# Optimization experiments

Measured on AMD Instinct MI355X. Metric: run time of the kernel, lower is better.

## Reference

```python
import jax, jax.numpy as jnp
import numpy as np
from math import sqrt

B, TS_D, SEG, D, H, FACTOR, DFF = 16, 32, 64, 256, 8, 10, 1024
EPS = 1e-3  # keras LayerNormalization default epsilon


def _dense_params(key, din, dout):
    return (jax.random.normal(key, (din, dout), jnp.float32) * 0.02,
            jnp.zeros((dout,), jnp.float32))


def setup_inputs() -> dict:
    key = jax.random.key(0)
    ks = jax.random.split(key, 32)
    inp = {"x": jax.random.normal(ks[0], (B, TS_D, SEG, D), jnp.float32)}
    inp["router"] = jax.random.normal(ks[1], (SEG, FACTOR, D), jnp.float32) * 0.02
    i = 2
    for pref in ["t", "s", "r"]:  # time_attention, dim_sender, dim_receiver
        for nm in ["q", "k", "v", "o"]:
            w, b = _dense_params(ks[i], D, D); i += 1
            inp[pref + nm + "_w"] = w
            inp[pref + nm + "_b"] = b
    for j in range(1, 5):
        inp["n%d_g" % j] = jnp.ones((D,), jnp.float32)
        inp["n%d_b" % j] = jnp.zeros((D,), jnp.float32)
    for pref in ["m1", "m2"]:
        w1, b1 = _dense_params(ks[i], D, DFF); i += 1
        w2, b2 = _dense_params(ks[i], DFF, D); i += 1
        inp[pref + "w1"] = w1; inp[pref + "b1"] = b1
        inp[pref + "w2"] = w2; inp[pref + "b2"] = b2
    return inp


def _attn(q, k, v, wq, bq, wk, bk, wv, bv, wo, bo):
    # multi-head full attention; dropout is identity at inference
    Bq, L, _ = q.shape
    S = k.shape[1]
    E = D // H
    qh = (q @ wq + bq).reshape(Bq, L, H, E)
    kh = (k @ wk + bk).reshape(Bq, S, H, E)
    vh = (v @ wv + bv).reshape(Bq, S, H, E)
    scores = jnp.einsum('blhe,bshe->bhls', qh, kh) * (1.0 / sqrt(E))
    A = jax.nn.softmax(scores, axis=-1)
    out = jnp.einsum('bhls,bshd->blhd', A, vh).reshape(Bq, L, H * E)
    return out @ wo + bo


def _ln(x, g, b):
    m = jnp.mean(x, axis=-1, keepdims=True)
    v = jnp.mean(jnp.square(x - m), axis=-1, keepdims=True)
    return (x - m) / jnp.sqrt(v + EPS) * g + b


def _mlp(x, w1, b1, w2, b2):
    return jax.nn.gelu(x @ w1 + b1, approximate=False) @ w2 + b2


def reference(x, router, tq_w, tq_b, tk_w, tk_b, tv_w, tv_b, to_w, to_b,
              sq_w, sq_b, sk_w, sk_b, sv_w, sv_b, so_w, so_b,
              rq_w, rq_b, rk_w, rk_b, rv_w, rv_b, ro_w, ro_b,
              n1_g, n1_b, n2_g, n2_b, n3_g, n3_b, n4_g, n4_b,
              m1w1, m1b1, m1w2, m1b2, m2w1, m2b1, m2w2, m2b2):
    b, ts_d, seg, d = x.shape
    # ---- stage 1: attention across time segments (per variable) ----
    time_in = x.reshape(b * ts_d, seg, d)
    time_enc = _attn(time_in, time_in, time_in,
                     tq_w, tq_b, tk_w, tk_b, tv_w, tv_b, to_w, to_b)
    dim_in = _ln(time_in + time_enc, n1_g, n1_b)
    dim_in = _ln(dim_in + _mlp(dim_in, m1w1, m1b1, m1w2, m1b2), n2_g, n2_b)
    # ---- stage 2: routed attention across variable dimension (per segment) ----
    # '(b ts_d) seg d -> (b seg) ts_d d'
    dim_send = dim_in.reshape(b, ts_d, seg, d).transpose(0, 2, 1, 3).reshape(b * seg, ts_d, d)
    # tf.repeat(router, repeats=batch, axis=0): each segment's router repeated b times (seg-major)
    batch_router = jnp.repeat(router, b, axis=0)  # (seg*b, factor, d)
    dim_buffer = _attn(batch_router, dim_send, dim_send,
                       sq_w, sq_b, sk_w, sk_b, sv_w, sv_b, so_w, so_b)
    dim_receive = _attn(dim_send, dim_buffer, dim_buffer,
                        rq_w, rq_b, rk_w, rk_b, rv_w, rv_b, ro_w, ro_b)
    dim_enc = _ln(dim_send + dim_receive, n3_g, n3_b)
    dim_enc = _ln(dim_enc + _mlp(dim_enc, m2w1, m2b1, m2w2, m2b2), n4_g, n4_b)
    # '(b seg) ts_d d -> b ts_d seg d'
    return dim_enc.reshape(b, seg, ts_d, d).transpose(0, 2, 1, 3)
```

## Files before the change

kernel.cpp:

```cpp
#include <hip/hip_runtime.h>
#include <hip/hip_bf16.h>

#define DIM   256
#define NH    8
#define HE    32
#define ROWS  32768
#define EPS_LN 1e-3f

typedef float f32x4 __attribute__((ext_vector_type(4)));
typedef short s16x8 __attribute__((ext_vector_type(8)));
typedef short s16x4 __attribute__((ext_vector_type(4)));
typedef __bf16 bf16x8 __attribute__((ext_vector_type(8)));

__device__ __forceinline__ unsigned short f2bf(float f){
    union { float f; unsigned int u; } v; v.f = f;
    unsigned int u = v.u;
    return (unsigned short)((u + 0x7fffu + ((u >> 16) & 1u)) >> 16);
}

__device__ __forceinline__ float gelu_f(float x){
    return 0.5f * x * (1.0f + erff(x * 0.70710678118654752440f));
}

__device__ __forceinline__ void mfma16i(f32x4& acc, s16x8 a, s16x8 b){
    acc = __builtin_amdgcn_mfma_f32_16x16x32_bf16(
        __builtin_bit_cast(bf16x8, a), __builtin_bit_cast(bf16x8, b), acc, 0, 0, 0);
}

__device__ __forceinline__ s16x8 pack8(float4 a, float4 b){
    s16x8 v;
    v[0]=(short)f2bf(a.x); v[1]=(short)f2bf(a.y);
    v[2]=(short)f2bf(a.z); v[3]=(short)f2bf(a.w);
    v[4]=(short)f2bf(b.x); v[5]=(short)f2bf(b.y);
    v[6]=(short)f2bf(b.z); v[7]=(short)f2bf(b.w);
    return v;
}

__device__ __forceinline__ void gld16(const unsigned short* g, unsigned short* l){
    __builtin_amdgcn_global_load_lds(
        (const __attribute__((address_space(1))) unsigned int*)g,
        (__attribute__((address_space(3))) unsigned int*)l, 16, 0, 0);
}

struct WtArgs { const float* w[16]; unsigned short* o[16]; };
__global__ __launch_bounds__(256) void transp_all_k(WtArgs a){
    int idx = blockIdx.x * 256 + threadIdx.x;
    int wi, rem, K, N;
    if (idx < 786432){ wi = idx >> 16; rem = idx & 65535; K = 256; N = 256; }
    else { int t = idx - 786432; wi = 12 + (t >> 18); rem = t & 262143;
           if ((wi & 1) == 0){ K = 256; N = 1024; } else { K = 1024; N = 256; } }
    int ln = (N == 256) ? 8 : 10;
    int k = rem >> ln, n = rem & (N - 1);
    a.o[wi][n * K + k] = f2bf(a.w[wi][rem]);
}

struct BcArgs { const float* src[8]; float* dst; };
__global__ __launch_bounds__(256) void bias_cat_k(BcArgs a){
    int idx = blockIdx.x * 256 + threadIdx.x;
    a.dst[idx] = a.src[idx >> 8][idx & 255];
}

template<int ACT, int ABF16, int CBF16, int SPLIT>
__global__ __launch_bounds__(256) void gemm_k(const void* __restrict__ Av,
        const unsigned short* __restrict__ Wt, const float* __restrict__ bias,
        void* C0, void* C1, void* C2, int M, int N, int K){
    __shared__ __align__(16) unsigned short As[2][128 * 32];
    __shared__ __align__(16) unsigned short Bs[2][128 * 32];
    const int tid  = threadIdx.x;
    const long row0 = (long)blockIdx.x * 128;
    const long col0 = (long)blockIdx.y * 128;
    const int w = tid >> 6, lane = tid & 63;
    const int wm = w >> 1, wn = w & 1;
    const int l15 = lane & 15, g = lane >> 4;
    const unsigned short* Bg = Wt + (size_t)(col0 + 32 * w + (lane >> 2)) * K + (lane & 3) * 8;
    const int sr = tid >> 1, sk = (tid & 1) << 4;
    const float* Ap = (const float*)Av + (size_t)(row0 + sr) * K + sk;
    const unsigned short* Ag = (const unsigned short*)Av +
        (size_t)(row0 + 32 * w + (lane >> 2)) * K + (lane & 3) * 8;

    auto stage = [&](int kk, int nb){
        gld16(Bg + kk, &Bs[nb][(32 * w) * 32]);
        gld16(Bg + 16 * K + kk, &Bs[nb][(32 * w + 16) * 32]);
        if (ABF16){
            gld16(Ag + kk, &As[nb][(32 * w) * 32]);
            gld16(Ag + 16 * K + kk, &As[nb][(32 * w + 16) * 32]);
        } else {
            float4 a0 = *(const float4*)(Ap + kk);
            float4 a1 = *(const float4*)(Ap + kk + 4);
            float4 a2 = *(const float4*)(Ap + kk + 8);
            float4 a3 = *(const float4*)(Ap + kk + 12);
            *(s16x8*)&As[nb][sr * 32 + sk]     = pack8(a0, a1);
            *(s16x8*)&As[nb][sr * 32 + sk + 8] = pack8(a2, a3);
        }
    };

    f32x4 acc[4][4];
    #pragma unroll
    for (int i = 0; i < 4; i++)
        #pragma unroll
        for (int jj = 0; jj < 4; jj++) acc[i][jj] = (f32x4){0,0,0,0};

    stage(0, 0);
    __syncthreads();
    int cur = 0;
    for (int k0 = 0; k0 < K; k0 += 32){
        if (k0 + 32 < K) stage(k0 + 32, cur ^ 1);
        s16x8 af[4], bf[4];
        #pragma unroll
        for (int mi = 0; mi < 4; mi++)
            af[mi] = *(const s16x8*)&As[cur][(wm * 64 + mi * 16 + l15) * 32 + g * 8];
        #pragma unroll
        for (int ni = 0; ni < 4; ni++)
            bf[ni] = *(const s16x8*)&Bs[cur][(wn * 64 + ni * 16 + l15) * 32 + g * 8];
        #pragma unroll
        for (int mi = 0; mi < 4; mi++)
            #pragma unroll
            for (int ni = 0; ni < 4; ni++)
                mfma16i(acc[mi][ni], af[mi], bf[ni]);
        __syncthreads();
        cur ^= 1;
    }
    const int sel = SPLIT ? (int)(col0 >> 8) : 0;
    void* Cp = SPLIT ? (sel == 0 ? C0 : (sel == 1 ? C1 : C2)) : C0;
    const int ldc = SPLIT ? 256 : N;
    float bb[4];
    #pragma unroll
    for (int ni = 0; ni < 4; ni++) bb[ni] = bias[col0 + wn * 64 + ni * 16 + l15];
    #pragma unroll
    for (int mi = 0; mi < 4; mi++){
        const long grow = row0 + wm * 64 + mi * 16 + g * 4;
        #pragma unroll
        for (int ni = 0; ni < 4; ni++){
            int gcol = (int)col0 + wn * 64 + ni * 16 + l15;
            int lcol = SPLIT ? (gcol & 255) : gcol;
            #pragma unroll
            for (int r = 0; r < 4; r++){
                float v = acc[mi][ni][r] + bb[ni];
                if (ACT) v = gelu_f(v);
                if (CBF16) ((unsigned short*)Cp)[(grow + r) * ldc + lcol] = f2bf(v);
                else       ((float*)Cp)[(grow + r) * ldc + lcol] = v;
            }
        }
    }
}

__global__ __launch_bounds__(64) void attn64_k(const float* __restrict__ Q,
        const float* __restrict__ Kp, const float* __restrict__ Vp,
        float* __restrict__ O){
    __shared__ __align__(16) unsigned short P[64][72];
    const int j = blockIdx.x >> 3, h = blockIdx.x & 7;
    const int lane = threadIdx.x;
    const int l15 = lane & 15, g = lane >> 4;
    const long base = (long)j * 64 * DIM;
    const int hoff = h * HE;
    const float scale = 0.17677669529663687f;
    s16x8 kf[4], qf[4];
    #pragma unroll
    for (int b = 0; b < 4; b++){
        const float* kp = Kp + base + (long)(b * 16 + l15) * DIM + hoff + g * 8;
        kf[b] = pack8(*(const float4*)kp, *(const float4*)(kp + 4));
        const float* qp = Q + base + (long)(b * 16 + l15) * DIM + hoff + g * 8;
        qf[b] = pack8(*(const float4*)qp, *(const float4*)(qp + 4));
    }
    f32x4 st[4][4];
    #pragma unroll
    for (int sb = 0; sb < 4; sb++)
        #pragma unroll
        for (int qb = 0; qb < 4; qb++) st[sb][qb] = (f32x4){0,0,0,0};
    #pragma unroll
    for (int sb = 0; sb < 4; sb++)
        #pragma unroll
        for (int qb = 0; qb < 4; qb++) mfma16i(st[sb][qb], kf[sb], qf[qb]);
    #pragma unroll
    for (int sb = 0; sb < 4; sb++)
        #pragma unroll
        for (int qb = 0; qb < 4; qb++)
            #pragma unroll
            for (int r = 0; r < 4; r++) st[sb][qb][r] *= scale;
    #pragma unroll
    for (int qb = 0; qb < 4; qb++){
        float mx = -1e30f;
        #pragma unroll
        for (int sb = 0; sb < 4; sb++)
            #pragma unroll
            for (int r = 0; r < 4; r++) mx = fmaxf(mx, st[sb][qb][r]);
        mx = fmaxf(mx, __shfl_xor(mx, 16, 64));
        mx = fmaxf(mx, __shfl_xor(mx, 32, 64));
        float sum = 0.f;
        #pragma unroll
        for (int sb = 0; sb < 4; sb++)
            #pragma unroll
            for (int r = 0; r < 4; r++){
                float e = expf(st[sb][qb][r] - mx);
                st[sb][qb][r] = e; sum += e;
            }
        sum += __shfl_xor(sum, 16, 64);
        sum += __shfl_xor(sum, 32, 64);
        float inv = 1.f / sum;
        const int q = qb * 16 + l15;
        #pragma unroll
        for (int sb = 0; sb < 4; sb++){
            s16x4 p4;
            #pragma unroll
            for (int r = 0; r < 4; r++) p4[r] = (short)f2bf(st[sb][qb][r] * inv);
            *(s16x4*)&P[q][sb * 16 + g * 4] = p4;
        }
    }
    __syncthreads();
    f32x4 o[4][2];
    #pragma unroll
    for (int qb = 0; qb < 4; qb++)
        #pragma unroll
        for (int eb = 0; eb < 2; eb++) o[qb][eb] = (f32x4){0,0,0,0};
    #pragma unroll
    for (int ksl = 0; ksl < 2; ksl++){
        s16x8 pf[4], vf[2];
        #pragma unroll
        for (int qb = 0; qb < 4; qb++)
            pf[qb] = *(const s16x8*)&P[qb * 16 + l15][ksl * 32 + g * 8];
        #pragma unroll
        for (int eb = 0; eb < 2; eb++){
            const float* vp = Vp + base + (long)(ksl * 32 + g * 8) * DIM + hoff + eb * 16 + l15;
            s16x8 vv;
            #pragma unroll
            for (int jj = 0; jj < 8; jj++) vv[jj] = (short)f2bf(vp[(long)jj * DIM]);
            vf[eb] = vv;
        }
        #pragma unroll
        for (int qb = 0; qb < 4; qb++)
            #pragma unroll
            for (int eb = 0; eb < 2; eb++) mfma16i(o[qb][eb], pf[qb], vf[eb]);
    }
    #pragma unroll
    for (int qb = 0; qb < 4; qb++)
        #pragma unroll
        for (int eb = 0; eb < 2; eb++){
            const int q = qb * 16 + g * 4;
            float* op = O + base + (long)q * DIM + hoff + eb * 16 + l15;
            #pragma unroll
            for (int r = 0; r < 4; r++) op[(long)r * DIM] = o[qb][eb][r];
        }
}

template<int L, int S, int QMODE>
__global__ __launch_bounds__(256) void attn_k(const float* __restrict__ Q,
        const float* __restrict__ Kp, const float* __restrict__ Vp,
        float* __restrict__ O){
    __shared__ float Qs[L][36];
    __shared__ float Ks[S][36];
    __shared__ float Vs[S][36];
    __shared__ float Sc[L][S + 1];
    const int j = blockIdx.x >> 3, h = blockIdx.x & 7;
    const int tid = threadIdx.x;
    const long qbase = QMODE ? (long)(j >> 4) * L : (long)j * L;
    const long kbase = (long)j * S;
    const long obase = (long)j * L;
    const int hoff = h * HE;
    for (int idx = tid; idx < L * 8; idx += 256){
        int i = idx >> 3, e4 = (idx & 7) << 2;
        *reinterpret_cast<float4*>(&Qs[i][e4]) =
            *reinterpret_cast<const float4*>(Q + (qbase + i) * DIM + hoff + e4);
    }
    for (int idx = tid; idx < S * 8; idx += 256){
        int i = idx >> 3, e4 = (idx & 7) << 2;
        *reinterpret_cast<float4*>(&Ks[i][e4]) =
            *reinterpret_cast<const float4*>(Kp + (kbase + i) * DIM + hoff + e4);
        *reinterpret_cast<float4*>(&Vs[i][e4]) =
            *reinterpret_cast<const float4*>(Vp + (kbase + i) * DIM + hoff + e4);
    }
    __syncthreads();
    for (int idx = tid; idx < L * S; idx += 256){
        int i = idx / S, jj = idx % S;
        float d = 0.f;
        #pragma unroll
        for (int q4 = 0; q4 < 8; q4++){
            float4 a = *reinterpret_cast<const float4*>(&Qs[i][q4 * 4]);
            float4 b = *reinterpret_cast<const float4*>(&Ks[jj][q4 * 4]);
            d += a.x * b.x + a.y * b.y + a.z * b.z + a.w * b.w;
        }
        Sc[i][jj] = d * 0.17677669529663687f;
    }
    __syncthreads();
    if (tid < L){
        float mx = -1e30f;
        for (int jj = 0; jj < S; jj++) mx = fmaxf(mx, Sc[tid][jj]);
        float s = 0.f;
        for (int jj = 0; jj < S; jj++){ float e = expf(Sc[tid][jj] - mx); Sc[tid][jj] = e; s += e; }
        float inv = 1.f / s;
        for (int jj = 0; jj < S; jj++) Sc[tid][jj] *= inv;
    }
    __syncthreads();
    for (int idx = tid; idx < L * 8; idx += 256){
        int i = idx >> 3, e4 = (idx & 7) << 2;
        float4 o = {0.f, 0.f, 0.f, 0.f};
        for (int jj = 0; jj < S; jj++){
            float s = Sc[i][jj];
            float4 v = *reinterpret_cast<const float4*>(&Vs[jj][e4]);
            o.x += s * v.x; o.y += s * v.y; o.z += s * v.z; o.w += s * v.w;
        }
        *reinterpret_cast<float4*>(O + (obase + i) * DIM + hoff + e4) = o;
    }
}

template<int PERM>
__global__ __launch_bounds__(256) void ln_k(const float* __restrict__ X,
        const float* __restrict__ R, const float* __restrict__ g,
        const float* __restrict__ be, float* __restrict__ Y){
    const int wid = threadIdx.x >> 6, lane = threadIdx.x & 63;
    const long row = (long)blockIdx.x * 4 + wid;
    float4 xv = *reinterpret_cast<const float4*>(X + row * DIM + lane * 4);
    float4 rv = *reinterpret_cast<const float4*>(R + row * DIM + lane * 4);
    float4 v = {xv.x + rv.x, xv.y + rv.y, xv.z + rv.z, xv.w + rv.w};
    float s = v.x + v.y + v.z + v.w;
    #pragma unroll
    for (int m = 1; m < 64; m <<= 1) s += __shfl_xor(s, m, 64);
    float mean = s * (1.f / 256.f);
    float dx = v.x - mean, dy = v.y - mean, dz = v.z - mean, dw = v.w - mean;
    float q = dx * dx + dy * dy + dz * dz + dw * dw;
    #pragma unroll
    for (int m = 1; m < 64; m <<= 1) q += __shfl_xor(q, m, 64);
    float rstd = rsqrtf(q * (1.f / 256.f) + EPS_LN);
    float4 gv = *reinterpret_cast<const float4*>(g  + lane * 4);
    float4 bv = *reinterpret_cast<const float4*>(be + lane * 4);
    long rout = row;
    if (PERM == 1){ int b = (int)(row >> 11), rem = (int)row & 2047, t = rem >> 6, sg = rem & 63;
                    rout = (long)b * 2048 + sg * 32 + t; }
    if (PERM == 2){ int b = (int)(row >> 11), rem = (int)row & 2047, sg = rem >> 5, t = rem & 31;
                    rout = (long)b * 2048 + t * 64 + sg; }
    float4 o = { dx * rstd * gv.x + bv.x, dy * rstd * gv.y + bv.y,
                 dz * rstd * gv.z + bv.z, dw * rstd * gv.w + bv.w };
    *reinterpret_cast<float4*>(Y + rout * DIM + lane * 4) = o;
}

extern "C" void kernel_launch(void* const* d_in, const int* in_sizes, int n_in,
                              void* d_out, int out_size, void* d_ws, size_t ws_size,
                              hipStream_t stream){
    const float* x      = (const float*)d_in[0];
    const float* router = (const float*)d_in[1];
    const float* n1g = (const float*)d_in[26]; const float* n1b = (const float*)d_in[27];
    const float* n2g = (const float*)d_in[28]; const float* n2b = (const float*)d_in[29];
    const float* n3g = (const float*)d_in[30]; const float* n3b = (const float*)d_in[31];
    const float* n4g = (const float*)d_in[32]; const float* n4b = (const float*)d_in[33];

    char* ws = (char*)d_ws;
    const size_t ACTB = (size_t)ROWS * DIM * 4;
    float* buf0 = (float*)(ws);
    float* buf1 = (float*)(ws + 1 * ACTB);
    float* buf2 = (float*)(ws + 2 * ACTB);
    float* buf3 = (float*)(ws + 3 * ACTB);
    float* buf4 = (float*)(ws + 4 * ACTB);
    float* buf5 = (float*)(ws + 5 * ACTB);
    unsigned short* bufH16 = (unsigned short*)buf0;
    size_t off = 6 * ACTB;
    float* bufS1 = (float*)(ws + off); off += (size_t)10240 * 256 * 4;
    float* bufS2 = (float*)(ws + off); off += (size_t)10240 * 256 * 4;
    float* bufR  = (float*)(ws + off); off += (size_t)640 * 256 * 4;
    float* bcat  = (float*)(ws + off); off += 2048 * 4;
    unsigned short* wtbase = (unsigned short*)(ws + off);

    const int wsel[16] = {2,4,6, 12,14,18, 20,22, 8,10,16,24, 34,36,38,40};
    unsigned short* wt[16];
    { size_t o = 0;
      for (int i = 0; i < 12; i++){ wt[i] = wtbase + o; o += 65536; }
      for (int i = 12; i < 16; i++){ wt[i] = wtbase + o; o += 262144; } }
    WtArgs wa;
    for (int i = 0; i < 16; i++){ wa.w[i] = (const float*)d_in[wsel[i]]; wa.o[i] = wt[i]; }
    transp_all_k<<<7168, 256, 0, stream>>>(wa);
    BcArgs ba;
    { const int bs[8] = {3,5,7, 13,15,19, 21,23};
      for (int i = 0; i < 8; i++) ba.src[i] = (const float*)d_in[bs[i]];
      ba.dst = bcat; }
    bias_cat_k<<<8, 256, 0, stream>>>(ba);

    const unsigned short *G0 = wt[0], *G1 = wt[3], *G2 = wt[6];
    const unsigned short *Wto = wt[8], *Wsq = wt[9], *Wso = wt[10], *Wro = wt[11];
    const unsigned short *Wm1a = wt[12], *Wm1b = wt[13], *Wm2a = wt[14], *Wm2b = wt[15];
    const float* b_to = (const float*)d_in[9];  const float* b_sq = (const float*)d_in[11];
    const float* b_so = (const float*)d_in[17]; const float* b_ro = (const float*)d_in[25];
    const float* m1b1 = (const float*)d_in[35]; const float* m1b2 = (const float*)d_in[37];
    const float* m2b1 = (const float*)d_in[39]; const float* m2b2 = (const float*)d_in[41];

    gemm_k<0,0,0,1><<<dim3(256,6), 256, 0, stream>>>(x, G0, bcat,
        buf0, buf1, buf2, ROWS, 768, 256);
    attn64_k<<<dim3(512 * 8), 64, 0, stream>>>(buf0, buf1, buf2, buf3);
    gemm_k<0,0,0,0><<<dim3(256,2), 256, 0, stream>>>(buf3, Wto, b_to,
        buf5, nullptr, nullptr, ROWS, 256, 256);
    ln_k<0><<<ROWS / 4, 256, 0, stream>>>(buf5, x, n1g, n1b, buf4);
    gemm_k<1,0,1,0><<<dim3(256,8), 256, 0, stream>>>(buf4, Wm1a, m1b1,
        bufH16, nullptr, nullptr, ROWS, 1024, 256);
    gemm_k<0,1,0,0><<<dim3(256,2), 256, 0, stream>>>(bufH16, Wm1b, m1b2,
        buf5, nullptr, nullptr, ROWS, 256, 1024);
    ln_k<1><<<ROWS / 4, 256, 0, stream>>>(buf5, buf4, n2g, n2b, buf0);

    gemm_k<0,0,0,0><<<dim3(5,2), 256, 0, stream>>>(router, Wsq, b_sq,
        bufR, nullptr, nullptr, 640, 256, 256);
    gemm_k<0,0,0,1><<<dim3(256,6), 256, 0, stream>>>(buf0, G1, bcat + 768,
        buf1, buf2, buf3, ROWS, 768, 256);
    attn_k<10,32,1><<<dim3(1024 * 8), 256, 0, stream>>>(bufR, buf1, buf2, bufS1);
    gemm_k<0,0,0,0><<<dim3(80,2), 256, 0, stream>>>(bufS1, Wso, b_so,
        bufS2, nullptr, nullptr, 10240, 256, 256);
    gemm_k<0,0,0,1><<<dim3(80,4), 256, 0, stream>>>(bufS2, G2, bcat + 1536,
        bufS1, buf1, nullptr, 10240, 512, 256);
    attn_k<32,10,0><<<dim3(1024 * 8), 256, 0, stream>>>(buf3, bufS1, buf1, buf2);
    gemm_k<0,0,0,0><<<dim3(256,2), 256, 0, stream>>>(buf2, Wro, b_ro,
        buf3, nullptr, nullptr, ROWS, 256, 256);
    ln_k<0><<<ROWS / 4, 256, 0, stream>>>(buf3, buf0, n3g, n3b, buf4);
    gemm_k<1,0,1,0><<<dim3(256,8), 256, 0, stream>>>(buf4, Wm2a, m2b1,
        bufH16, nullptr, nullptr, ROWS, 1024, 256);
    gemm_k<0,1,0,0><<<dim3(256,2), 256, 0, stream>>>(bufH16, Wm2b, m2b2,
        buf5, nullptr, nullptr, ROWS, 256, 1024);
    ln_k<2><<<ROWS / 4, 256, 0, stream>>>(buf5, buf4, n4g, n4b, (float*)d_out);
}
```

Measured before the change: 617.7 us.

## Store all intermediate activations in bf16 and swizzle GEMM LDS tiles

Every intermediate activation buffer (QKV projections, attention outputs, LayerNorm outputs, GEMM outputs) is now stored in bf16 instead of fp32. This roughly halves activation memory traffic between the many kernels, and the input x and router are converted to bf16 once up front. The GEMM now always loads A directly to LDS via global_load_lds, uses an XOR swizzle to avoid bank conflicts, and replaces __syncthreads with explicit vmcnt waits and s_barrier. The added bf16 rounding of residuals and LayerNorm inputs reduces accuracy.

```diff
diff --git a/kernel.cpp b/kernel.cpp
--- a/kernel.cpp
+++ b/kernel.cpp
@@ -17,29 +17,32 @@
     unsigned int u = v.u;
     return (unsigned short)((u + 0x7fffu + ((u >> 16) & 1u)) >> 16);
 }
-
+__device__ __forceinline__ float bf2f(unsigned short u){
+    union { unsigned int i; float f; } v; v.i = (unsigned int)u << 16; return v.f;
+}
 __device__ __forceinline__ float gelu_f(float x){
     return 0.5f * x * (1.0f + erff(x * 0.70710678118654752440f));
 }
-
 __device__ __forceinline__ void mfma16i(f32x4& acc, s16x8 a, s16x8 b){
     acc = __builtin_amdgcn_mfma_f32_16x16x32_bf16(
         __builtin_bit_cast(bf16x8, a), __builtin_bit_cast(bf16x8, b), acc, 0, 0, 0);
 }
-
-__device__ __forceinline__ s16x8 pack8(float4 a, float4 b){
-    s16x8 v;
-    v[0]=(short)f2bf(a.x); v[1]=(short)f2bf(a.y);
-    v[2]=(short)f2bf(a.z); v[3]=(short)f2bf(a.w);
-    v[4]=(short)f2bf(b.x); v[5]=(short)f2bf(b.y);
-    v[6]=(short)f2bf(b.z); v[7]=(short)f2bf(b.w);
-    return v;
-}
-
 __device__ __forceinline__ void gld16(const unsigned short* g, unsigned short* l){
     __builtin_amdgcn_global_load_lds(
         (const __attribute__((address_space(1))) unsigned int*)g,
         (__attribute__((address_space(3))) unsigned int*)l, 16, 0, 0);
+}
+
+__global__ __launch_bounds__(256) void conv_k(const float* __restrict__ in,
+        unsigned short* __restrict__ out, int n8){
+    int idx = blockIdx.x * 256 + threadIdx.x;
+    if (idx >= n8) return;
+    const float4 a = *(const float4*)(in + idx * 8);
+    const float4 b = *(const float4*)(in + idx * 8 + 4);
+    s16x8 v;
+    v[0]=(short)f2bf(a.x); v[1]=(short)f2bf(a.y); v[2]=(short)f2bf(a.z); v[3]=(short)f2bf(a.w);
+    v[4]=(short)f2bf(b.x); v[5]=(short)f2bf(b.y); v[6]=(short)f2bf(b.z); v[7]=(short)f2bf(b.w);
+    *(s16x8*)(out + idx * 8) = v;
 }
 
 struct WtArgs { const float* w[16]; unsigned short* o[16]; };
@@ -60,10 +63,11 @@
     a.dst[idx] = a.src[idx >> 8][idx & 255];
 }
 
-template<int ACT, int ABF16, int CBF16, int SPLIT>
-__global__ __launch_bounds__(256) void gemm_k(const void* __restrict__ Av,
+template<int ACT, int SPLIT>
+__global__ __launch_bounds__(256) void gemm_k(const unsigned short* __restrict__ A,
         const unsigned short* __restrict__ Wt, const float* __restrict__ bias,
-        void* C0, void* C1, void* C2, int M, int N, int K){
+        unsigned short* C0, unsigned short* C1, unsigned short* C2,
+        int M, int N, int K){
     __shared__ __align__(16) unsigned short As[2][128 * 32];
     __shared__ __align__(16) unsigned short Bs[2][128 * 32];
     const int tid  = threadIdx.x;
@@ -72,56 +76,55 @@
     const int w = tid >> 6, lane = tid & 63;
     const int wm = w >> 1, wn = w & 1;
     const int l15 = lane & 15, g = lane >> 4;
-    const unsigned short* Bg = Wt + (size_t)(col0 + 32 * w + (lane >> 2)) * K + (lane & 3) * 8;
-    const int sr = tid >> 1, sk = (tid & 1) << 4;
-    const float* Ap = (const float*)Av + (size_t)(row0 + sr) * K + sk;
-    const unsigned short* Ag = (const unsigned short*)Av +
-        (size_t)(row0 + 32 * w + (lane >> 2)) * K + (lane & 3) * 8;
-
-    auto stage = [&](int kk, int nb){
-        gld16(Bg + kk, &Bs[nb][(32 * w) * 32]);
-        gld16(Bg + 16 * K + kk, &Bs[nb][(32 * w + 16) * 32]);
-        if (ABF16){
-            gld16(Ag + kk, &As[nb][(32 * w) * 32]);
-            gld16(Ag + 16 * K + kk, &As[nb][(32 * w + 16) * 32]);
+    const int jsrc = ((lane & 3) ^ ((lane >> 3) & 3)) * 8;
+    const unsigned short* Ag = A  + (size_t)(row0 + 32 * w + (lane >> 2)) * K + jsrc;
+    const unsigned short* Bg = Wt + (size_t)(col0 + 32 * w + (lane >> 2)) * K + jsrc;
+    unsigned short* Al0[2] = { &As[0][(32 * w) * 32], &As[1][(32 * w) * 32] };
+    unsigned short* Bl0[2] = { &Bs[0][(32 * w) * 32], &Bs[1][(32 * w) * 32] };
+
+    f32x4 acc[4][4];
+    #pragma unroll
+    for (int i = 0; i < 4; i++)
+        #pragma unroll
+        for (int jj = 0; jj < 4; jj++) acc[i][jj] = (f32x4){0,0,0,0};
+
+    const int NT = K >> 5;
+    gld16(Ag, Al0[0]);          gld16(Ag + 16 * K, Al0[0] + 16 * 32);
+    gld16(Bg, Bl0[0]);          gld16(Bg + 16 * K, Bl0[0] + 16 * 32);
+    for (int t = 0; t < NT; ++t){
+        const int cur = t & 1;
+        if (t + 1 < NT){
+            const int kk = (t + 1) << 5;
+            gld16(Ag + kk, Al0[cur ^ 1]);  gld16(Ag + kk + 16 * K, Al0[cur ^ 1] + 16 * 32);
+            gld16(Bg + kk, Bl0[cur ^ 1]);  gld16(Bg + kk + 16 * K, Bl0[cur ^ 1] + 16 * 32);
+            asm volatile("s_waitcnt vmcnt(4)" ::: "memory");
         } else {
-            float4 a0 = *(const float4*)(Ap + kk);
-            float4 a1 = *(const float4*)(Ap + kk + 4);
-            float4 a2 = *(const float4*)(Ap + kk + 8);
-            float4 a3 = *(const float4*)(Ap + kk + 12);
-            *(s16x8*)&As[nb][sr * 32 + sk]     = pack8(a0, a1);
-            *(s16x8*)&As[nb][sr * 32 + sk + 8] = pack8(a2, a3);
-        }
-    };
-
-    f32x4 acc[4][4];
-    #pragma unroll
-    for (int i = 0; i < 4; i++)
-        #pragma unroll
-        for (int jj = 0; jj < 4; jj++) acc[i][jj] = (f32x4){0,0,0,0};
-
-    stage(0, 0);
-    __syncthreads();
-    int cur = 0;
-    for (int k0 = 0; k0 < K; k0 += 32){
-        if (k0 + 32 < K) stage(k0 + 32, cur ^ 1);
+            asm volatile("s_waitcnt vmcnt(0)" ::: "memory");
+        }
+        __builtin_amdgcn_sched_barrier(0);
+        __builtin_amdgcn_s_barrier();
+        __builtin_amdgcn_sched_barrier(0);
         s16x8 af[4], bf[4];
         #pragma unroll
-        for (int mi = 0; mi < 4; mi++)
-            af[mi] = *(const s16x8*)&As[cur][(wm * 64 + mi * 16 + l15) * 32 + g * 8];
-        #pragma unroll
-        for (int ni = 0; ni < 4; ni++)
-            bf[ni] = *(const s16x8*)&Bs[cur][(wn * 64 + ni * 16 + l15) * 32 + g * 8];
+        for (int mi = 0; mi < 4; mi++){
+            const int r = mi * 16 + l15;
+            af[mi] = *(const s16x8*)&As[cur][(wm * 64 + r) * 32 + ((g ^ ((l15 >> 1) & 3)) * 8)];
+        }
+        #pragma unroll
+        for (int ni = 0; ni < 4; ni++){
+            const int r = ni * 16 + l15;
+            bf[ni] = *(const s16x8*)&Bs[cur][(wn * 64 + r) * 32 + ((g ^ ((l15 >> 1) & 3)) * 8)];
+        }
         #pragma unroll
         for (int mi = 0; mi < 4; mi++)
             #pragma unroll
             for (int ni = 0; ni < 4; ni++)
                 mfma16i(acc[mi][ni], af[mi], bf[ni]);
-        __syncthreads();
-        cur ^= 1;
+        __builtin_amdgcn_sched_barrier(0);
+        __builtin_amdgcn_s_barrier();
     }
     const int sel = SPLIT ? (int)(col0 >> 8) : 0;
-    void* Cp = SPLIT ? (sel == 0 ? C0 : (sel == 1 ? C1 : C2)) : C0;
+    unsigned short* Cp = SPLIT ? (sel == 0 ? C0 : (sel == 1 ? C1 : C2)) : C0;
     const int ldc = SPLIT ? 256 : N;
     float bb[4];
     #pragma unroll
@@ -137,16 +140,15 @@
             for (int r = 0; r < 4; r++){
                 float v = acc[mi][ni][r] + bb[ni];
                 if (ACT) v = gelu_f(v);
-                if (CBF16) ((unsigned short*)Cp)[(grow + r) * ldc + lcol] = f2bf(v);
-                else       ((float*)Cp)[(grow + r) * ldc + lcol] = v;
+                Cp[(grow + r) * ldc + lcol] = f2bf(v);
             }
         }
     }
 }
 
-__global__ __launch_bounds__(64) void attn64_k(const float* __restrict__ Q,
-        const float* __restrict__ Kp, const float* __restrict__ Vp,
-        float* __restrict__ O){
+__global__ __launch_bounds__(64) void attn64_k(const unsigned short* __restrict__ Q,
+        const unsigned short* __restrict__ Kp, const unsigned short* __restrict__ Vp,
+        unsigned short* __restrict__ O){
     __shared__ __align__(16) unsigned short P[64][72];
     const int j = blockIdx.x >> 3, h = blockIdx.x & 7;
     const int lane = threadIdx.x;
@@ -157,10 +159,8 @@
     s16x8 kf[4], qf[4];
     #pragma unroll
     for (int b = 0; b < 4; b++){
-        const float* kp = Kp + base + (long)(b * 16 + l15) * DIM + hoff + g * 8;
-        kf[b] = pack8(*(const float4*)kp, *(const float4*)(kp + 4));
-        const float* qp = Q + base + (long)(b * 16 + l15) * DIM + hoff + g * 8;
-        qf[b] = pack8(*(const float4*)qp, *(const float4*)(qp + 4));
+        kf[b] = *(const s16x8*)(Kp + base + (long)(b * 16 + l15) * DIM + hoff + g * 8);
+        qf[b] = *(const s16x8*)(Q  + base + (long)(b * 16 + l15) * DIM + hoff + g * 8);
     }
     f32x4 st[4][4];
     #pragma unroll
@@ -220,10 +220,10 @@
             pf[qb] = *(const s16x8*)&P[qb * 16 + l15][ksl * 32 + g * 8];
         #pragma unroll
         for (int eb = 0; eb < 2; eb++){
-            const float* vp = Vp + base + (long)(ksl * 32 + g * 8) * DIM + hoff + eb * 16 + l15;
+            const unsigned short* vp = Vp + base + (long)(ksl * 32 + g * 8) * DIM + hoff + eb * 16 + l15;
             s16x8 vv;
             #pragma unroll
-            for (int jj = 0; jj < 8; jj++) vv[jj] = (short)f2bf(vp[(long)jj * DIM]);
+            for (int jj = 0; jj < 8; jj++) vv[jj] = (short)vp[(long)jj * DIM];
             vf[eb] = vv;
         }
         #pragma unroll
@@ -236,16 +236,16 @@
         #pragma unroll
         for (int eb = 0; eb < 2; eb++){
             const int q = qb * 16 + g * 4;
-            float* op = O + base + (long)q * DIM + hoff + eb * 16 + l15;
-            #pragma unroll
-            for (int r = 0; r < 4; r++) op[(long)r * DIM] = o[qb][eb][r];
+            unsigned short* op = O + base + (long)q * DIM + hoff + eb * 16 + l15;
+            #pragma unroll
+            for (int r = 0; r < 4; r++) op[(long)r * DIM] = f2bf(o[qb][eb][r]);
         }
 }
 
 template<int L, int S, int QMODE>
-__global__ __launch_bounds__(256) void attn_k(const float* __restrict__ Q,
-        const float* __restrict__ Kp, const float* __restrict__ Vp,
-        float* __restrict__ O){
+__global__ __launch_bounds__(256) void attn_k(const unsigned short* __restrict__ Q,
+        const unsigned short* __restrict__ Kp, const unsigned short* __restrict__ Vp,
+        unsigned short* __restrict__ O){
     __shared__ float Qs[L][36];
     __shared__ float Ks[S][36];
     __shared__ float Vs[S][36];
@@ -256,17 +256,21 @@
     const long kbase = (long)j * S;
     const long obase = (long)j * L;
     const int hoff = h * HE;
-    for (int idx = tid; idx < L * 8; idx += 256){
-        int i = idx >> 3, e4 = (idx & 7) << 2;
-        *reinterpret_cast<float4*>(&Qs[i][e4]) =
-            *reinterpret_cast<const float4*>(Q + (qbase + i) * DIM + hoff + e4);
-    }
-    for (int idx = tid; idx < S * 8; idx += 256){
-        int i = idx >> 3, e4 = (idx & 7) << 2;
-        *reinterpret_cast<float4*>(&Ks[i][e4]) =
-            *reinterpret_cast<const float4*>(Kp + (kbase + i) * DIM + hoff + e4);
-        *reinterpret_cast<float4*>(&Vs[i][e4]) =
-            *reinterpret_cast<const float4*>(Vp + (kbase + i) * DIM + hoff + e4);
+    for (int idx = tid; idx < L * 4; idx += 256){
+        int i = idx >> 2, e8 = (idx & 3) * 8;
+        s16x8 v = *(const s16x8*)(Q + (qbase + i) * DIM + hoff + e8);
+        #pragma unroll
+        for (int t = 0; t < 8; t++) Qs[i][e8 + t] = bf2f((unsigned short)v[t]);
+    }
+    for (int idx = tid; idx < S * 4; idx += 256){
+        int i = idx >> 2, e8 = (idx & 3) * 8;
+        s16x8 vk = *(const s16x8*)(Kp + (kbase + i) * DIM + hoff + e8);
+        s16x8 vv = *(const s16x8*)(Vp + (kbase + i) * DIM + hoff + e8);
+        #pragma unroll
+        for (int t = 0; t < 8; t++){
+            Ks[i][e8 + t] = bf2f((unsigned short)vk[t]);
+            Vs[i][e8 + t] = bf2f((unsigned short)vv[t]);
+        }
     }
     __syncthreads();
     for (int idx = tid; idx < L * S; idx += 256){
@@ -298,19 +302,25 @@
             float4 v = *reinterpret_cast<const float4*>(&Vs[jj][e4]);
             o.x += s * v.x; o.y += s * v.y; o.z += s * v.z; o.w += s * v.w;
         }
-        *reinterpret_cast<float4*>(O + (obase + i) * DIM + hoff + e4) = o;
-    }
-}
-
-template<int PERM>
-__global__ __launch_bounds__(256) void ln_k(const float* __restrict__ X,
-        const float* __restrict__ R, const float* __restrict__ g,
-        const float* __restrict__ be, float* __restrict__ Y){
+        s16x4 p;
+        p[0] = (short)f2bf(o.x); p[1] = (short)f2bf(o.y);
+        p[2] = (short)f2bf(o.z); p[3] = (short)f2bf(o.w);
+        *(s16x4*)(O + (obase + i) * DIM + hoff + e4) = p;
+    }
+}
+
+template<int PERM, int OUTF32>
+__global__ __launch_bounds__(256) void ln_k(const unsigned short* __restrict__ X,
+        const unsigned short* __restrict__ R, const float* __restrict__ g,
+        const float* __restrict__ be, void* __restrict__ Y){
     const int wid = threadIdx.x >> 6, lane = threadIdx.x & 63;
     const long row = (long)blockIdx.x * 4 + wid;
-    float4 xv = *reinterpret_cast<const float4*>(X + row * DIM + lane * 4);
-    float4 rv = *reinterpret_cast<const float4*>(R + row * DIM + lane * 4);
-    float4 v = {xv.x + rv.x, xv.y + rv.y, xv.z + rv.z, xv.w + rv.w};
+    s16x4 xv4 = *(const s16x4*)(X + row * DIM + lane * 4);
+    s16x4 rv4 = *(const s16x4*)(R + row * DIM + lane * 4);
+    float4 v = { bf2f((unsigned short)xv4[0]) + bf2f((unsigned short)rv4[0]),
+                 bf2f((unsigned short)xv4[1]) + bf2f((unsigned short)rv4[1]),
+                 bf2f((unsigned short)xv4[2]) + bf2f((unsigned short)rv4[2]),
+                 bf2f((unsigned short)xv4[3]) + bf2f((unsigned short)rv4[3]) };
     float s = v.x + v.y + v.z + v.w;
     #pragma unroll
     for (int m = 1; m < 64; m <<= 1) s += __shfl_xor(s, m, 64);
@@ -329,7 +339,14 @@
                     rout = (long)b * 2048 + t * 64 + sg; }
     float4 o = { dx * rstd * gv.x + bv.x, dy * rstd * gv.y + bv.y,
                  dz * rstd * gv.z + bv.z, dw * rstd * gv.w + bv.w };
-    *reinterpret_cast<float4*>(Y + rout * DIM + lane * 4) = o;
+    if (OUTF32){
+        *reinterpret_cast<float4*>((float*)Y + rout * DIM + lane * 4) = o;
+    } else {
+        s16x4 p;
+        p[0] = (short)f2bf(o.x); p[1] = (short)f2bf(o.y);
+        p[2] = (short)f2bf(o.z); p[3] = (short)f2bf(o.w);
+        *(s16x4*)((unsigned short*)Y + rout * DIM + lane * 4) = p;
+    }
 }
 
 extern "C" void kernel_launch(void* const* d_in, const int* in_sizes, int n_in,
@@ -343,19 +360,21 @@
     const float* n4g = (const float*)d_in[32]; const float* n4b = (const float*)d_in[33];
 
     char* ws = (char*)d_ws;
-    const size_t ACTB = (size_t)ROWS * DIM * 4;
-    float* buf0 = (float*)(ws);
-    float* buf1 = (float*)(ws + 1 * ACTB);
-    float* buf2 = (float*)(ws + 2 * ACTB);
-    float* buf3 = (float*)(ws + 3 * ACTB);
-    float* buf4 = (float*)(ws + 4 * ACTB);
-    float* buf5 = (float*)(ws + 5 * ACTB);
-    unsigned short* bufH16 = (unsigned short*)buf0;
-    size_t off = 6 * ACTB;
-    float* bufS1 = (float*)(ws + off); off += (size_t)10240 * 256 * 4;
-    float* bufS2 = (float*)(ws + off); off += (size_t)10240 * 256 * 4;
-    float* bufR  = (float*)(ws + off); off += (size_t)640 * 256 * 4;
-    float* bcat  = (float*)(ws + off); off += 2048 * 4;
+    const size_t ACT2 = (size_t)ROWS * DIM * 2;
+    unsigned short* x16  = (unsigned short*)(ws);
+    unsigned short* buf0 = (unsigned short*)(ws + 1 * ACT2);
+    unsigned short* buf1 = (unsigned short*)(ws + 2 * ACT2);
+    unsigned short* buf2 = (unsigned short*)(ws + 3 * ACT2);
+    unsigned short* buf3 = (unsigned short*)(ws + 4 * ACT2);
+    unsigned short* buf4 = (unsigned short*)(ws + 5 * ACT2);
+    unsigned short* buf5 = (unsigned short*)(ws + 6 * ACT2);
+    size_t off = 7 * ACT2;
+    unsigned short* bufH = (unsigned short*)(ws + off); off += (size_t)ROWS * 1024 * 2;
+    unsigned short* bufS1 = (unsigned short*)(ws + off); off += (size_t)10240 * 256 * 2;
+    unsigned short* bufS2 = (unsigned short*)(ws + off); off += (size_t)10240 * 256 * 2;
+    unsigned short* r16   = (unsigned short*)(ws + off); off += (size_t)640 * 256 * 2;
+    unsigned short* bufRt = (unsigned short*)(ws + off); off += (size_t)640 * 256 * 2;
+    float* bcat = (float*)(ws + off); off += 2048 * 4;
     unsigned short* wtbase = (unsigned short*)(ws + off);
 
     const int wsel[16] = {2,4,6, 12,14,18, 20,22, 8,10,16,24, 34,36,38,40};
@@ -371,6 +390,8 @@
       for (int i = 0; i < 8; i++) ba.src[i] = (const float*)d_in[bs[i]];
       ba.dst = bcat; }
     bias_cat_k<<<8, 256, 0, stream>>>(ba);
+    conv_k<<<(ROWS * DIM / 8 + 255) / 256, 256, 0, stream>>>(x, x16, ROWS * DIM / 8);
+    conv_k<<<(640 * 256 / 8 + 255) / 256, 256, 0, stream>>>(router, r16, 640 * 256 / 8);
 
     const unsigned short *G0 = wt[0], *G1 = wt[3], *G2 = wt[6];
     const unsigned short *Wto = wt[8], *Wsq = wt[9], *Wso = wt[10], *Wro = wt[11];
@@ -380,34 +401,34 @@
     const float* m1b1 = (const float*)d_in[35]; const float* m1b2 = (const float*)d_in[37];
     const float* m2b1 = (const float*)d_in[39]; const float* m2b2 = (const float*)d_in[41];
 
-    gemm_k<0,0,0,1><<<dim3(256,6), 256, 0, stream>>>(x, G0, bcat,
+    gemm_k<0,1><<<dim3(256,6), 256, 0, stream>>>(x16, G0, bcat,
         buf0, buf1, buf2, ROWS, 768, 256);
     attn64_k<<<dim3(512 * 8), 64, 0, stream>>>(buf0, buf1, buf2, buf3);
-    gemm_k<0,0,0,0><<<dim3(256,2), 256, 0, stream>>>(buf3, Wto, b_to,
+    gemm_k<0,0><<<dim3(256,2), 256, 0, stream>>>(buf3, Wto, b_to,
         buf5, nullptr, nullptr, ROWS, 256, 256);
-    ln_k<0><<<ROWS / 4, 256, 0, stream>>>(buf5, x, n1g, n1b, buf4);
-    gemm_k<1,0,1,0><<<dim3(256,8), 256, 0, stream>>>(buf4, Wm1a, m1b1,
-        bufH16, nullptr, nullptr, ROWS, 1024, 256);
-    gemm_k<0,1,0,0><<<dim3(256,2), 256, 0, stream>>>(bufH16, Wm1b, m1b2,
+    ln_k<0,0><<<ROWS / 4, 256, 0, stream>>>(buf5, x16, n1g, n1b, buf4);
+    gemm_k<1,0><<<dim3(256,8), 256, 0, stream>>>(buf4, Wm1a, m1b1,
+        bufH, nullptr, nullptr, ROWS, 1024, 256);
+    gemm_k<0,0><<<dim3(256,2), 256, 0, stream>>>(bufH, Wm1b, m1b2,
         buf5, nullptr, nullptr, ROWS, 256, 1024);
-    ln_k<1><<<ROWS / 4, 256, 0, stream>>>(buf5, buf4, n2g, n2b, buf0);
-
-    gemm_k<0,0,0,0><<<dim3(5,2), 256, 0, stream>>>(router, Wsq, b_sq,
-        bufR, nullptr, nullptr, 640, 256, 256);
-    gemm_k<0,0,0,1><<<dim3(256,6), 256, 0, stream>>>(buf0, G1, bcat + 768,
+    ln_k<1,0><<<ROWS / 4, 256, 0, stream>>>(buf5, buf4, n2g, n2b, buf0);
+
+    gemm_k<0,0><<<dim3(5,2), 256, 0, stream>>>(r16, Wsq, b_sq,
+        bufRt, nullptr, nullptr, 640, 256, 256);
+    gemm_k<0,1><<<dim3(256,6), 256, 0, stream>>>(buf0, G1, bcat + 768,
         buf1, buf2, buf3, ROWS, 768, 256);
-    attn_k<10,32,1><<<dim3(1024 * 8), 256, 0, stream>>>(bufR, buf1, buf2, bufS1);
-    gemm_k<0,0,0,0><<<dim3(80,2), 256, 0, stream>>>(bufS1, Wso, b_so,
+    attn_k<10,32,1><<<dim3(1024 * 8), 256, 0, stream>>>(bufRt, buf1, buf2, bufS1);
+    gemm_k<0,0><<<dim3(80,2), 256, 0, stream>>>(bufS1, Wso, b_so,
         bufS2, nullptr, nullptr, 10240, 256, 256);
-    gemm_k<0,0,0,1><<<dim3(80,4), 256, 0, stream>>>(bufS2, G2, bcat + 1536,
+    gemm_k<0,1><<<dim3(80,4), 256, 0, stream>>>(bufS2, G2, bcat + 1536,
         bufS1, buf1, nullptr, 10240, 512, 256);
     attn_k<32,10,0><<<dim3(1024 * 8), 256, 0, stream>>>(buf3, bufS1, buf1, buf2);
-    gemm_k<0,0,0,0><<<dim3(256,2), 256, 0, stream>>>(buf2, Wro, b_ro,
+    gemm_k<0,0><<<dim3(256,2), 256, 0, stream>>>(buf2, Wro, b_ro,
         buf3, nullptr, nullptr, ROWS, 256, 256);
-    ln_k<0><<<ROWS / 4, 256, 0, stream>>>(buf3, buf0, n3g, n3b, buf4);
-    gemm_k<1,0,1,0><<<dim3(256,8), 256, 0, stream>>>(buf4, Wm2a, m2b1,
-        bufH16, nullptr, nullptr, ROWS, 1024, 256);
-    gemm_k<0,1,0,0><<<dim3(256,2), 256, 0, stream>>>(bufH16, Wm2b, m2b2,
+    ln_k<0,0><<<ROWS / 4, 256, 0, stream>>>(buf3, buf0, n3g, n3b, buf4);
+    gemm_k<1,0><<<dim3(256,8), 256, 0, stream>>>(buf4, Wm2a, m2b1,
+        bufH, nullptr, nullptr, ROWS, 1024, 256);
+    gemm_k<0,0><<<dim3(256,2), 256, 0, stream>>>(bufH, Wm2b, m2b2,
         buf5, nullptr, nullptr, ROWS, 256, 1024);
-    ln_k<2><<<ROWS / 4, 256, 0, stream>>>(buf5, buf4, n4g, n4b, (float*)d_out);
-}
+    ln_k<2,1><<<ROWS / 4, 256, 0, stream>>>(buf5, buf4, n4g, n4b, (float*)d_out);
+}
```

After: 524.9 us. -15.0%, faster.
